# Performance work log

Hardware: AMD Instinct MI355X
Metric: run time of the kernel (lower is better)

## Reference

```python
import jax, jax.numpy as jnp
import numpy as np

B, QL, CL = 4, 256, 512
XD, ED, DIM, YD = 128, 128, 128, 16


def setup_inputs() -> dict:
    key = jax.random.key(0)
    ks = jax.random.split(key, 9)
    s = lambda fan_in: 1.0 / np.sqrt(fan_in)
    return {
        "q": jax.random.normal(ks[0], (B, QL, XD), jnp.float32),
        "f_embed": jax.random.normal(ks[1], (B, CL, ED), jnp.float32),
        "att_logits": jax.random.normal(ks[2], (B, QL, CL), jnp.float32),
        # layer 1 of concat-MLP, split into per-branch blocks (same math as concat@W1)
        "W1q": jax.random.normal(ks[3], (XD, DIM), jnp.float32) * s(XD + ED),
        "W1f": jax.random.normal(ks[4], (ED, DIM), jnp.float32) * s(XD + ED),
        "b1": jnp.zeros((DIM,), jnp.float32),
        "W2": jax.random.normal(ks[5], (DIM, DIM), jnp.float32) * s(DIM),
        "b2": jnp.zeros((DIM,), jnp.float32),
        "Wout": jax.random.normal(ks[6], (DIM, 2 * YD), jnp.float32) * s(DIM),
        "bout": jnp.zeros((2 * YD,), jnp.float32),
    }


def reference(q, f_embed, att_logits, W1q, W1f, b1, W2, b2, Wout, bout):
    # First layer: concat([tile(q), tile(f)]) @ W1 == q@W1q (+) f@W1f broadcast-added.
    qp = jnp.einsum("bqd,dh->bqh", q, W1q)            # [B,Q,H]
    fp = jnp.einsum("bcd,dh->bch", f_embed, W1f)      # [B,C,H]
    h = jax.nn.relu(qp[:, :, None, :] + fp[:, None, :, :] + b1)   # [B,Q,C,H]
    h = jax.nn.relu(jnp.einsum("bqch,hk->bqck", h, W2) + b2)      # [B,Q,C,H]
    out = jnp.einsum("bqch,hy->bqcy", h, Wout) + bout             # [B,Q,C,2Y]
    mu, s = jnp.split(out, 2, axis=-1)                            # [B,Q,C,Y] each
    sigma = jax.nn.softplus(jnp.maximum(-15.0, s))
    # MixtureSameFamily(Categorical(att_logits), MVNDiag(mu, sigma)).sample()
    kcat, keps = jax.random.split(jax.random.key(1))
    idx = jax.random.categorical(kcat, att_logits, axis=-1)       # [B,Q]
    gather = lambda t: jnp.take_along_axis(t, idx[:, :, None, None], axis=2)[:, :, 0, :]
    mu_sel, sig_sel = gather(mu), gather(sigma)                   # [B,Q,Y]
    eps = jax.random.normal(keps, mu_sel.shape, mu_sel.dtype)
    y_hat = mu_sel + sig_sel * eps                                # [B,Q,Y]
    return y_hat
```

## Files before the change

kernel.cpp:

```cpp
#include <hip/hip_runtime.h>
#include <stdint.h>

#define Bc   4
#define QLc  256
#define CLc  512
#define Dc   128
#define YDc  16
#define NROW (Bc * QLc)

__device__ __forceinline__ uint32_t rotl32(uint32_t x, int d) {
  return (x << d) | (x >> (32 - d));
}

__device__ __forceinline__ void tf2x32(uint32_t k0, uint32_t k1, uint32_t x0,
                                       uint32_t x1, uint32_t& o0, uint32_t& o1) {
  const uint32_t k2 = k0 ^ k1 ^ 0x1BD11BDAu;
  uint32_t v0 = x0 + k0, v1 = x1 + k1;
  v0 += v1; v1 = rotl32(v1, 13); v1 ^= v0;
  v0 += v1; v1 = rotl32(v1, 15); v1 ^= v0;
  v0 += v1; v1 = rotl32(v1, 26); v1 ^= v0;
  v0 += v1; v1 = rotl32(v1, 6);  v1 ^= v0;
  v0 += k1; v1 += k2 + 1u;
  v0 += v1; v1 = rotl32(v1, 17); v1 ^= v0;
  v0 += v1; v1 = rotl32(v1, 29); v1 ^= v0;
  v0 += v1; v1 = rotl32(v1, 16); v1 ^= v0;
  v0 += v1; v1 = rotl32(v1, 24); v1 ^= v0;
  v0 += k2; v1 += k0 + 2u;
  v0 += v1; v1 = rotl32(v1, 13); v1 ^= v0;
  v0 += v1; v1 = rotl32(v1, 15); v1 ^= v0;
  v0 += v1; v1 = rotl32(v1, 26); v1 ^= v0;
  v0 += v1; v1 = rotl32(v1, 6);  v1 ^= v0;
  v0 += k0; v1 += k1 + 3u;
  v0 += v1; v1 = rotl32(v1, 17); v1 ^= v0;
  v0 += v1; v1 = rotl32(v1, 29); v1 ^= v0;
  v0 += v1; v1 = rotl32(v1, 16); v1 ^= v0;
  v0 += v1; v1 = rotl32(v1, 24); v1 ^= v0;
  v0 += k1; v1 += k2 + 4u;
  v0 += v1; v1 = rotl32(v1, 13); v1 ^= v0;
  v0 += v1; v1 = rotl32(v1, 15); v1 ^= v0;
  v0 += v1; v1 = rotl32(v1, 26); v1 ^= v0;
  v0 += v1; v1 = rotl32(v1, 6);  v1 ^= v0;
  v0 += k2; v1 += k0 + 5u;
  o0 = v0; o1 = v1;
}

__device__ __forceinline__ void subkeys(uint32_t& ck0, uint32_t& ck1,
                                        uint32_t& ek0, uint32_t& ek1) {
  tf2x32(0u, 1u, 0u, 0u, ck0, ck1);
  tf2x32(0u, 1u, 0u, 1u, ek0, ek1);
}

__device__ __forceinline__ uint32_t rbits(uint32_t k0, uint32_t k1, uint32_t i) {
  uint32_t o0, o1;
  tf2x32(k0, k1, 0u, i, o0, o1);
  return o0 ^ o1;
}

__device__ __forceinline__ float bits_to_unit(uint32_t bits) {
  return __uint_as_float((bits >> 9) | 0x3f800000u) - 1.0f;
}

__device__ __forceinline__ float erfinv_f(float x) {
  float w = -logf((1.0f - x) * (1.0f + x));
  float p;
  if (w < 5.0f) {
    w -= 2.5f;
    p = 2.81022636e-08f;
    p = fmaf(p, w, 3.43273939e-07f);
    p = fmaf(p, w, -3.5233877e-06f);
    p = fmaf(p, w, -4.39150654e-06f);
    p = fmaf(p, w, 0.00021858087f);
    p = fmaf(p, w, -0.00125372503f);
    p = fmaf(p, w, -0.00417768164f);
    p = fmaf(p, w, 0.246640727f);
    p = fmaf(p, w, 1.50140941f);
  } else {
    w = sqrtf(w) - 3.0f;
    p = -0.000200214257f;
    p = fmaf(p, w, 0.000100950558f);
    p = fmaf(p, w, 0.00134934322f);
    p = fmaf(p, w, -0.00367342844f);
    p = fmaf(p, w, 0.00573950773f);
    p = fmaf(p, w, -0.0076224613f);
    p = fmaf(p, w, 0.00943887047f);
    p = fmaf(p, w, 1.00167406f);
    p = fmaf(p, w, 2.83297682f);
  }
  return p * x;
}

__global__ __launch_bounds__(256) void k_fused(
    const float* __restrict__ q, const float* __restrict__ f,
    const float* __restrict__ logits, const float* __restrict__ W1q,
    const float* __restrict__ W1f, const float* __restrict__ b1,
    const float* __restrict__ W2, const float* __restrict__ b2,
    const float* __restrict__ Wout, const float* __restrict__ bout,
    float* __restrict__ out) {
  const int tid = threadIdx.x;
  const int r   = tid >> 7;
  const int l   = tid & 127;
  const int row = blockIdx.x * 2 + r;
  const int b   = row >> 8;

  __shared__ float sx[2][Dc];
  __shared__ float sh[2][Dc];
  __shared__ float sv[256];
  __shared__ int   si[256];
  __shared__ float spart[2][4][32];
  __shared__ float so[2][32];
  __shared__ int   sc[2];

  const float qv = q[row * Dc + l];

  uint32_t ck0, ck1, ek0, ek1;
  subkeys(ck0, ck1, ek0, ek1);

  float best = -3.4e38f;
  int bi = 1 << 30;
#pragma unroll
  for (int j = 0; j < 4; ++j) {
    const int c = l + j * 128;
    const uint32_t i = (uint32_t)(row * CLc + c);
    const uint32_t bits = rbits(ck0, ck1, i);
    const float fl = bits_to_unit(bits);
    const float u = fmaxf(1.17549435e-38f, fl);
    const float g = -logf(-logf(u));
    const float val = g + logits[i];
    if (val > best || (val == best && c < bi)) { best = val; bi = c; }
  }
  sv[tid] = best; si[tid] = bi;
  __syncthreads();
  for (int s = 64; s > 0; s >>= 1) {
    if (l < s) {
      const int a0 = r * 128 + l, a1 = a0 + s;
      const float v2 = sv[a1];
      const int i2 = si[a1];
      if (v2 > sv[a0] || (v2 == sv[a0] && i2 < si[a0])) {
        sv[a0] = v2; si[a0] = i2;
      }
    }
    __syncthreads();
  }
  if (l == 0) sc[r] = si[r * 128];

  sx[r][l] = qv;
  __syncthreads();
  float acc1 = 0.0f;
  for (int h = 0; h < Dc; ++h) acc1 = fmaf(sx[r][h], W1q[h * Dc + l], acc1);

  const int csel = sc[r];
  const float fv = f[(b * CLc + csel) * Dc + l];
  __syncthreads();
  sx[r][l] = fv;
  __syncthreads();
  float accf = 0.0f;
  for (int h = 0; h < Dc; ++h) accf = fmaf(sx[r][h], W1f[h * Dc + l], accf);

  sh[r][l] = fmaxf(acc1 + accf + b1[l], 0.0f);
  __syncthreads();

  float acc2 = b2[l];
  for (int h = 0; h < Dc; ++h) acc2 = fmaf(sh[r][h], W2[h * Dc + l], acc2);
  __syncthreads();
  sh[r][l] = fmaxf(acc2, 0.0f);
  __syncthreads();

  {
    const int k  = tid & 31;
    const int rr = (tid >> 5) & 1;
    const int g  = tid >> 6;
    float p = 0.0f;
#pragma unroll
    for (int hh = 0; hh < 32; ++hh) {
      const int h = g * 32 + hh;
      p = fmaf(sh[rr][h], Wout[h * 32 + k], p);
    }
    spart[rr][g][k] = p;
  }
  __syncthreads();
  if (tid < 64) {
    const int rr = tid >> 5, k = tid & 31;
    so[rr][k] = bout[k] + spart[rr][0][k] + spart[rr][1][k] +
                spart[rr][2][k] + spart[rr][3][k];
  }
  __syncthreads();

  if (tid < 32) {
    const int rr = tid >> 4, y = tid & 15;
    const int orow = blockIdx.x * 2 + rr;
    const float mu = so[rr][y];
    const float s  = so[rr][16 + y];
    const float sm = fmaxf(-15.0f, s);
    const float sigma = fmaxf(sm, 0.0f) + log1pf(expf(-fabsf(sm)));

    const uint32_t i = (uint32_t)(orow * YDc + y);
    const uint32_t bits = rbits(ek0, ek1, i);
    const float fl = bits_to_unit(bits);
    const float lo = -0.999999940395355224609375f;
    const float prod = __fmul_rn(fl, 2.0f);
    const float u = fmaxf(lo, __fadd_rn(prod, lo));
    const float eps = 1.4142135623730951f * erfinv_f(u);
    out[orow * YDc + y] = mu + sigma * eps;
  }
}

extern "C" void kernel_launch(void* const* d_in, const int* in_sizes, int n_in,
                              void* d_out, int out_size, void* d_ws, size_t ws_size,
                              hipStream_t stream) {
  const float* q      = (const float*)d_in[0];
  const float* f      = (const float*)d_in[1];
  const float* logits = (const float*)d_in[2];
  const float* W1q    = (const float*)d_in[3];
  const float* W1f    = (const float*)d_in[4];
  const float* b1     = (const float*)d_in[5];
  const float* W2     = (const float*)d_in[6];
  const float* b2     = (const float*)d_in[7];
  const float* Wout   = (const float*)d_in[8];
  const float* bout   = (const float*)d_in[9];
  float* out = (float*)d_out;

  k_fused<<<dim3(NROW / 2), dim3(256), 0, stream>>>(
      q, f, logits, W1q, W1f, b1, W2, b2, Wout, bout, out);
}
```

Before: 84.59 us.

## Process four rows per block and use wave shuffles for categorical argmax

Each block now handles four query rows instead of two. Each thread accumulates two rows per weight load, so the global weight traffic per row for W1q, W1f and W2 is halved. The Gumbel argmax now runs one wavefront per row and reduces with xor shuffles instead of a shared-memory tree that needed a barrier at every step. The grid is halved to 256 blocks, which may leave part of the device underused.

```diff
diff --git a/kernel.cpp b/kernel.cpp
--- a/kernel.cpp
+++ b/kernel.cpp
@@ -7,6 +7,7 @@
 #define Dc   128
 #define YDc  16
 #define NROW (Bc * QLc)
+#define RPB  4
 
 __device__ __forceinline__ uint32_t rotl32(uint32_t x, int d) {
   return (x << d) | (x >> (32 - d));
@@ -96,98 +97,113 @@
     const float* __restrict__ W2, const float* __restrict__ b2,
     const float* __restrict__ Wout, const float* __restrict__ bout,
     float* __restrict__ out) {
-  const int tid = threadIdx.x;
-  const int r   = tid >> 7;
-  const int l   = tid & 127;
-  const int row = blockIdx.x * 2 + r;
-  const int b   = row >> 8;
-
-  __shared__ float sx[2][Dc];
-  __shared__ float sh[2][Dc];
-  __shared__ float sv[256];
-  __shared__ int   si[256];
-  __shared__ float spart[2][4][32];
-  __shared__ float so[2][32];
-  __shared__ int   sc[2];
-
-  const float qv = q[row * Dc + l];
+  const int tid  = threadIdx.x;
+  const int row0 = blockIdx.x * RPB;
+
+  __shared__ float sx[RPB][Dc];
+  __shared__ float sh[RPB][Dc];
+  __shared__ float spart[RPB][2][32];
+  __shared__ float so[RPB][32];
+  __shared__ int   sc[RPB];
 
   uint32_t ck0, ck1, ek0, ek1;
   subkeys(ck0, ck1, ek0, ek1);
 
-  float best = -3.4e38f;
-  int bi = 1 << 30;
-#pragma unroll
-  for (int j = 0; j < 4; ++j) {
-    const int c = l + j * 128;
-    const uint32_t i = (uint32_t)(row * CLc + c);
-    const uint32_t bits = rbits(ck0, ck1, i);
-    const float fl = bits_to_unit(bits);
-    const float u = fmaxf(1.17549435e-38f, fl);
-    const float g = -logf(-logf(u));
-    const float val = g + logits[i];
-    if (val > best || (val == best && c < bi)) { best = val; bi = c; }
-  }
-  sv[tid] = best; si[tid] = bi;
-  __syncthreads();
-  for (int s = 64; s > 0; s >>= 1) {
-    if (l < s) {
-      const int a0 = r * 128 + l, a1 = a0 + s;
-      const float v2 = sv[a1];
-      const int i2 = si[a1];
-      if (v2 > sv[a0] || (v2 == sv[a0] && i2 < si[a0])) {
-        sv[a0] = v2; si[a0] = i2;
-      }
+  {
+    const int wv   = tid >> 6;
+    const int lane = tid & 63;
+    const int row  = row0 + wv;
+    float best = -3.4e38f;
+    int bi = 1 << 30;
+#pragma unroll
+    for (int j = 0; j < 8; ++j) {
+      const int c = lane + j * 64;
+      const uint32_t i = (uint32_t)(row * CLc + c);
+      const uint32_t bits = rbits(ck0, ck1, i);
+      const float fl = bits_to_unit(bits);
+      const float u = fmaxf(1.17549435e-38f, fl);
+      const float g = -logf(-logf(u));
+      const float val = g + logits[i];
+      if (val > best || (val == best && c < bi)) { best = val; bi = c; }
     }
-    __syncthreads();
-  }
-  if (l == 0) sc[r] = si[r * 128];
-
-  sx[r][l] = qv;
-  __syncthreads();
-  float acc1 = 0.0f;
-  for (int h = 0; h < Dc; ++h) acc1 = fmaf(sx[r][h], W1q[h * Dc + l], acc1);
-
-  const int csel = sc[r];
-  const float fv = f[(b * CLc + csel) * Dc + l];
-  __syncthreads();
-  sx[r][l] = fv;
-  __syncthreads();
-  float accf = 0.0f;
-  for (int h = 0; h < Dc; ++h) accf = fmaf(sx[r][h], W1f[h * Dc + l], accf);
-
-  sh[r][l] = fmaxf(acc1 + accf + b1[l], 0.0f);
-  __syncthreads();
-
-  float acc2 = b2[l];
-  for (int h = 0; h < Dc; ++h) acc2 = fmaf(sh[r][h], W2[h * Dc + l], acc2);
-  __syncthreads();
-  sh[r][l] = fmaxf(acc2, 0.0f);
+#pragma unroll
+    for (int s = 32; s > 0; s >>= 1) {
+      const float ov = __shfl_xor(best, s);
+      const int   oi = __shfl_xor(bi, s);
+      if (ov > best || (ov == best && oi < bi)) { best = ov; bi = oi; }
+    }
+    if (lane == 0) sc[wv] = bi;
+  }
+
+#pragma unroll
+  for (int i = tid; i < RPB * Dc; i += 256)
+    sx[i >> 7][i & 127] = q[(row0 + (i >> 7)) * Dc + (i & 127)];
+  __syncthreads();
+
+  const int l    = tid & 127;
+  const int half = tid >> 7;
+  const int r0 = half * 2, r1 = half * 2 + 1;
+  float accq0 = 0.f, accq1 = 0.f;
+  for (int h = 0; h < Dc; ++h) {
+    const float w = W1q[h * Dc + l];
+    accq0 = fmaf(sx[r0][h], w, accq0);
+    accq1 = fmaf(sx[r1][h], w, accq1);
+  }
+  __syncthreads();
+
+#pragma unroll
+  for (int i = tid; i < RPB * Dc; i += 256) {
+    const int rr = i >> 7;
+    const int b = (row0 + rr) >> 8;
+    sx[rr][i & 127] = f[(b * CLc + sc[rr]) * Dc + (i & 127)];
+  }
+  __syncthreads();
+  float accf0 = 0.f, accf1 = 0.f;
+  for (int h = 0; h < Dc; ++h) {
+    const float w = W1f[h * Dc + l];
+    accf0 = fmaf(sx[r0][h], w, accf0);
+    accf1 = fmaf(sx[r1][h], w, accf1);
+  }
+
+  const float bias1 = b1[l];
+  sh[r0][l] = fmaxf(accq0 + accf0 + bias1, 0.0f);
+  sh[r1][l] = fmaxf(accq1 + accf1 + bias1, 0.0f);
+  __syncthreads();
+
+  const float bias2 = b2[l];
+  float acc20 = bias2, acc21 = bias2;
+  for (int h = 0; h < Dc; ++h) {
+    const float w = W2[h * Dc + l];
+    acc20 = fmaf(sh[r0][h], w, acc20);
+    acc21 = fmaf(sh[r1][h], w, acc21);
+  }
+  __syncthreads();
+  sh[r0][l] = fmaxf(acc20, 0.0f);
+  sh[r1][l] = fmaxf(acc21, 0.0f);
   __syncthreads();
 
   {
     const int k  = tid & 31;
-    const int rr = (tid >> 5) & 1;
-    const int g  = tid >> 6;
+    const int rr = (tid >> 5) & 3;
+    const int g  = tid >> 7;
     float p = 0.0f;
 #pragma unroll
-    for (int hh = 0; hh < 32; ++hh) {
-      const int h = g * 32 + hh;
+    for (int hh = 0; hh < 64; ++hh) {
+      const int h = g * 64 + hh;
       p = fmaf(sh[rr][h], Wout[h * 32 + k], p);
     }
     spart[rr][g][k] = p;
   }
   __syncthreads();
-  if (tid < 64) {
+  if (tid < 128) {
     const int rr = tid >> 5, k = tid & 31;
-    so[rr][k] = bout[k] + spart[rr][0][k] + spart[rr][1][k] +
-                spart[rr][2][k] + spart[rr][3][k];
-  }
-  __syncthreads();
-
-  if (tid < 32) {
+    so[rr][k] = bout[k] + spart[rr][0][k] + spart[rr][1][k];
+  }
+  __syncthreads();
+
+  if (tid < RPB * YDc) {
     const int rr = tid >> 4, y = tid & 15;
-    const int orow = blockIdx.x * 2 + rr;
+    const int orow = row0 + rr;
     const float mu = so[rr][y];
     const float s  = so[rr][16 + y];
     const float sm = fmaxf(-15.0f, s);
@@ -219,6 +235,6 @@
   const float* bout   = (const float*)d_in[9];
   float* out = (float*)d_out;
 
-  k_fused<<<dim3(NROW / 2), dim3(256), 0, stream>>>(
+  k_fused<<<dim3(NROW / RPB), dim3(256), 0, stream>>>(
       q, f, logits, W1q, W1f, b1, W2, b2, Wout, bout, out);
 }
```

Result: slower. 90.58 us (+7.1%).
